# Kernel optimization log

Hardware: AMD Instinct MI355X
Metric: run time of the kernel (lower is better)

The kernel has to match this reference:

```python
import jax, jax.numpy as jnp
import numpy as np

B, L, T = 2048, 512, 32


def setup_inputs() -> dict:
    key = jax.random.key(0)
    k1, k2, k3, k4 = jax.random.split(key, 4)
    emit_score = jax.random.normal(k1, (B, L, T), dtype=jnp.float32)
    transition = jax.random.normal(k2, (T, T), dtype=jnp.float32)
    tags = jax.random.randint(k3, (B, L), 0, T, dtype=jnp.int32)
    lengths = jax.random.randint(k4, (B,), 1, L + 1, dtype=jnp.int32)
    return {"emit_score": emit_score, "transition": transition,
            "tags": tags, "lengths": lengths}


def reference(emit_score, transition, tags, lengths):
    # CRF negative log-likelihood (calculate_loss), per-example loss [B].
    b, l, t = emit_score.shape
    mask = jnp.arange(l)[None, :] < lengths[:, None]          # [B,L] bool
    maskf = mask.astype(emit_score.dtype)

    # --- gold path score ---
    gold = jnp.take_along_axis(emit_score, tags[:, :, None], axis=2)[..., 0]  # [B,L]
    trans_gold = transition[tags[:, :-1], tags[:, 1:]]        # [B,L-1]
    gold = gold.at[:, 1:].add(trans_gold)
    total_score = (gold * maskf).sum(axis=1)                  # [B]

    # --- forward algorithm (log partition) via scan over time ---
    emit_tbT = jnp.transpose(emit_score, (1, 0, 2))           # [L,B,T]
    mask_tb = mask.T                                          # [L,B]

    def step(d, x):
        e_t, m_t = x                                          # [B,T], [B]
        # scores[b, prev, next] = d[b,prev] + transition[prev,next] + e_t[b,next]
        scores = d[:, :, None] + transition[None, :, :] + e_t[:, None, :]
        new_d = jax.nn.logsumexp(scores, axis=1)              # [B,T]
        d = jnp.where(m_t[:, None], new_d, d)                 # freeze finished rows
        return d, None

    d0 = emit_tbT[0]                                          # [B,T]
    d, _ = jax.lax.scan(step, d0, (emit_tbT[1:], mask_tb[1:]))
    log_z = jax.nn.logsumexp(d, axis=1)                       # [B]

    return log_z - total_score                                # loss = -llk
```

## Files before the change

### kernel.cpp

```cpp
#include <hip/hip_runtime.h>


constexpr int TT = 32;
constexpr int LL = 512;

#define L2E  1.4426950408889634f
#define LN2f 0.6931471805599453f

template<int I>
__device__ __forceinline__ float bcastf(float v) {
  return __int_as_float(__builtin_amdgcn_ds_swizzle(__float_as_int(v), (I << 5)));
}
template<int X>
__device__ __forceinline__ float swzxf(float v) {
  return __int_as_float(__builtin_amdgcn_ds_swizzle(__float_as_int(v), (X << 10) | 0x1F));
}

__global__ __launch_bounds__(64) void crf_fwd(
    const float* __restrict__ emit, const float* __restrict__ trans,
    const int* __restrict__ tags, const int* __restrict__ lengths,
    float* __restrict__ out, int B)
{
  __shared__ float  s_trans[TT * TT];
  __shared__ float4 s_alpha[2][TT / 4];

  {
    const float4* t4 = (const float4*)trans;
    float4* st4 = (float4*)s_trans;
#pragma unroll
    for (int k = 0; k < 4; ++k)
      st4[threadIdx.x + 64 * k] = t4[threadIdx.x + 64 * k];
  }
  __syncthreads();

  const int lane = threadIdx.x & 31;
  const int grp  = threadIdx.x >> 5;
  const int b = blockIdx.x * 2 + grp;
  if (b >= B) return;
  float* sa = (float*)&s_alpha[grp][0];

  float Ec[TT];
#pragma unroll
  for (int i = 0; i < TT; ++i)
    Ec[i] = __builtin_amdgcn_exp2f(s_trans[i * TT + lane] * L2E);

  const int len = lengths[b];
  const float* erow = emit + (size_t)b * (LL * TT);
  const int*  trow  = tags + (size_t)b * LL;

  float e0   = erow[lane];
  int   ptag = trow[0];
  float a    = __builtin_amdgcn_exp2f(e0 * L2E);
  float gacc = (lane == ptag) ? e0 : 0.f;
  float LS   = 0.f;

  int mlen = max(len, __shfl_xor(len, 32));
  mlen = __builtin_amdgcn_readfirstlane(mlen);
  const int nch = (mlen - 1 + 3) >> 2;

  float eb[4], en[4];
  int   tg[4], tgn[4];
#pragma unroll
  for (int k = 0; k < 4; ++k) {
    int t = 1 + k; int tc = t < LL ? t : LL - 1;
    eb[k] = erow[tc * TT + lane];
    tg[k] = trow[tc];
  }
#pragma unroll
  for (int k = 0; k < 4; ++k) {
    int t = 5 + k; int tc = t < LL ? t : LL - 1;
    en[k] = erow[tc * TT + lane];
    tgn[k] = trow[tc];
  }

  for (int c = 0; c < nch; ++c) {
    const int tb = 1 + (c << 2);

    float ep[4]; int tgp[4];
#pragma unroll
    for (int k = 0; k < 4; ++k) {
      int t = tb + 8 + k; int tc = t < LL ? t : LL - 1;
      ep[k]  = erow[tc * TT + lane];
      tgp[k] = trow[tc];
    }

    float e2v[4];
#pragma unroll
    for (int k = 0; k < 4; ++k) e2v[k] = __builtin_amdgcn_exp2f(eb[k] * L2E);

#pragma unroll
    for (int k = 0; k < 4; ++k) {
      const int t = tb + k;

      sa[lane] = a;
      float4 A[8];
#pragma unroll
      for (int q = 0; q < 8; ++q) A[q] = s_alpha[grp][q];

      float acc0 = 0.f, acc1 = 0.f, acc2 = 0.f, acc3 = 0.f;
#pragma unroll
      for (int q = 0; q < 8; ++q) {
        acc0 = fmaf(A[q].x, Ec[4 * q + 0], acc0);
        acc1 = fmaf(A[q].y, Ec[4 * q + 1], acc1);
        acc2 = fmaf(A[q].z, Ec[4 * q + 2], acc2);
        acc3 = fmaf(A[q].w, Ec[4 * q + 3], acc3);
      }
      float anew = ((acc0 + acc1) + (acc2 + acc3)) * e2v[k];
      const bool valid = t < len;
      a = valid ? anew : a;

      int tag  = tg[k];
      float tr = s_trans[(ptag << 5) + lane];
      gacc += ((lane == tag) && valid) ? (eb[k] + tr) : 0.f;
      ptag = tag;
    }

    float m = fmaxf(bcastf<0>(a), 1e-30f);
    float r = __builtin_amdgcn_rcpf(m);
    a *= r;
    LS += __builtin_amdgcn_logf(m);

#pragma unroll
    for (int k = 0; k < 4; ++k) {
      eb[k] = en[k]; tg[k] = tgn[k];
      en[k] = ep[k]; tgn[k] = tgp[k];
    }
  }

  float s  = a;
  float gs = gacc;
  s += swzxf<1>(s);   gs += swzxf<1>(gs);
  s += swzxf<2>(s);   gs += swzxf<2>(gs);
  s += swzxf<4>(s);   gs += swzxf<4>(gs);
  s += swzxf<8>(s);   gs += swzxf<8>(gs);
  s += swzxf<16>(s);  gs += swzxf<16>(gs);

  float logz = (__builtin_amdgcn_logf(s) + LS) * LN2f;
  if (lane == 0) out[b] = logz - gs;
}

extern "C" void kernel_launch(void* const* d_in, const int* in_sizes, int n_in,
                              void* d_out, int out_size, void* d_ws, size_t ws_size,
                              hipStream_t stream) {
  const float* emit    = (const float*)d_in[0];
  const float* trans   = (const float*)d_in[1];
  const int*   tags    = (const int*)d_in[2];
  const int*   lengths = (const int*)d_in[3];
  float*       out     = (float*)d_out;
  const int B = in_sizes[3];
  const int blocks = (B + 1) / 2;
  hipLaunchKernelGGL(crf_fwd, dim3(blocks), dim3(64), 0, stream,
                     emit, trans, tags, lengths, out, B);
}
```

Measured before the change: 273.2 us.

## Split each row's 32x32 matvec across a full wave using DPP broadcasts

Each 64-lane wave now handles one sequence instead of two. Every step's 32x32 recurrence is split into 16-wide halves that are combined with permlane16/permlane32 swaps. Source values are broadcast with DPP row broadcasts, which replaces the per-step LDS store and reload of alpha. Lanes alternate between two layouts on even and odd steps, and the emission prefetch is deepened by one chunk. This shortens the serial dependency chain per timestep, at the cost of twice as many waves and more register state.

```diff
diff --git a/kernel.cpp b/kernel.cpp
--- a/kernel.cpp
+++ b/kernel.cpp
@@ -7,135 +7,174 @@
 #define L2E  1.4426950408889634f
 #define LN2f 0.6931471805599453f
 
-template<int I>
-__device__ __forceinline__ float bcastf(float v) {
-  return __int_as_float(__builtin_amdgcn_ds_swizzle(__float_as_int(v), (I << 5)));
+#define DPPBC(b, vv) __int_as_float(__builtin_amdgcn_update_dpp( \
+    0, __float_as_int(vv), 0x150 + (b), 0xF, 0xF, false))
+
+__device__ __forceinline__ float swap16(float v, int lane) {
+#if __has_builtin(__builtin_amdgcn_permlane16_swap)
+  auto p = __builtin_amdgcn_permlane16_swap(__float_as_uint(v), __float_as_uint(v),
+                                            false, false);
+  return __uint_as_float((lane & 16) ? p[0] : p[1]);
+#else
+  return __int_as_float(__builtin_amdgcn_ds_swizzle(__float_as_int(v), 0x401F));
+#endif
 }
-template<int X>
-__device__ __forceinline__ float swzxf(float v) {
-  return __int_as_float(__builtin_amdgcn_ds_swizzle(__float_as_int(v), (X << 10) | 0x1F));
+
+__device__ __forceinline__ float swap32(float v, int lane) {
+#if __has_builtin(__builtin_amdgcn_permlane32_swap)
+  auto p = __builtin_amdgcn_permlane32_swap(__float_as_uint(v), __float_as_uint(v),
+                                            false, false);
+  return __uint_as_float((lane & 32) ? p[0] : p[1]);
+#else
+  return __int_as_float(__builtin_amdgcn_ds_bpermute((lane ^ 32) << 2,
+                                                     __float_as_int(v)));
+#endif
 }
+
+#define DO_FMAS(EC) \
+  acc0 = DPPBC(0, av)  * EC[0];            \
+  acc1 = DPPBC(1, av)  * EC[1];            \
+  acc2 = DPPBC(2, av)  * EC[2];            \
+  acc3 = DPPBC(3, av)  * EC[3];            \
+  acc0 = fmaf(DPPBC(4, av),  EC[4],  acc0); \
+  acc1 = fmaf(DPPBC(5, av),  EC[5],  acc1); \
+  acc2 = fmaf(DPPBC(6, av),  EC[6],  acc2); \
+  acc3 = fmaf(DPPBC(7, av),  EC[7],  acc3); \
+  acc0 = fmaf(DPPBC(8, av),  EC[8],  acc0); \
+  acc1 = fmaf(DPPBC(9, av),  EC[9],  acc1); \
+  acc2 = fmaf(DPPBC(10, av), EC[10], acc2); \
+  acc3 = fmaf(DPPBC(11, av), EC[11], acc3); \
+  acc0 = fmaf(DPPBC(12, av), EC[12], acc0); \
+  acc1 = fmaf(DPPBC(13, av), EC[13], acc1); \
+  acc2 = fmaf(DPPBC(14, av), EC[14], acc2); \
+  acc3 = fmaf(DPPBC(15, av), EC[15], acc3);
+
+#define STEP(k, PH) do {                                            \
+    const int t = tb + (k);                                         \
+    float acc0, acc1, acc2, acc3;                                   \
+    if (PH == 0) { DO_FMAS(EcQ) } else { DO_FMAS(EcR) }             \
+    float accs = (acc0 + acc1) + (acc2 + acc3);                     \
+    float oth  = (PH == 0) ? swap16(accs, lane) : swap32(accs, lane);\
+    float sum  = accs + oth;                                        \
+    float anew = sum * e2v[k];                                      \
+    const bool valid = t < len;                                     \
+    av = valid ? anew : av;                                         \
+    int tagk = tg[k];                                               \
+    const int jc = (PH == 0) ? jcolQ : jcolR;                       \
+    float tr = s_trans[(ptag << 5) + jc];                           \
+    const bool gm = (PH == 0) ? ((lane & 16) == 0) : (lane < 32);   \
+    gacc += (valid && gm && (jc == tagk)) ? (eb[k] + tr) : 0.f;     \
+    ptag = tagk;                                                    \
+  } while (0)
 
 __global__ __launch_bounds__(64) void crf_fwd(
     const float* __restrict__ emit, const float* __restrict__ trans,
     const int* __restrict__ tags, const int* __restrict__ lengths,
     float* __restrict__ out, int B)
 {
-  __shared__ float  s_trans[TT * TT];
-  __shared__ float4 s_alpha[2][TT / 4];
-
+  __shared__ float s_trans[TT * TT];
   {
     const float4* t4 = (const float4*)trans;
-    float4* st4 = (float4*)s_trans;
+    float4* st = (float4*)s_trans;
 #pragma unroll
     for (int k = 0; k < 4; ++k)
-      st4[threadIdx.x + 64 * k] = t4[threadIdx.x + 64 * k];
+      st[threadIdx.x + 64 * k] = t4[threadIdx.x + 64 * k];
   }
   __syncthreads();
 
-  const int lane = threadIdx.x & 31;
-  const int grp  = threadIdx.x >> 5;
-  const int b = blockIdx.x * 2 + grp;
+  const int lane = threadIdx.x & 63;
+  const int j16  = lane & 15;
+  const int bit4 = (lane >> 4) & 1;
+  const int bit5 = (lane >> 5) & 1;
+  const int b = blockIdx.x;
   if (b >= B) return;
-  float* sa = (float*)&s_alpha[grp][0];
 
-  float Ec[TT];
+  const int iQ    = 16 * bit4 + j16;
+  const int jcolQ = 16 * bit5 + j16;
+  const int jcolR = 16 * bit4 + j16;
+
+  float EcQ[16], EcR[16];
 #pragma unroll
-  for (int i = 0; i < TT; ++i)
-    Ec[i] = __builtin_amdgcn_exp2f(s_trans[i * TT + lane] * L2E);
+  for (int i = 0; i < 16; ++i) {
+    EcQ[i] = __builtin_amdgcn_exp2f(s_trans[(16 * bit4 + i) * TT + jcolQ] * L2E);
+    EcR[i] = __builtin_amdgcn_exp2f(s_trans[(16 * bit5 + i) * TT + jcolR] * L2E);
+  }
 
   const int len = lengths[b];
   const float* erow = emit + (size_t)b * (LL * TT);
   const int*  trow  = tags + (size_t)b * LL;
 
-  float e0   = erow[lane];
+  float e0   = erow[iQ];
   int   ptag = trow[0];
-  float a    = __builtin_amdgcn_exp2f(e0 * L2E);
-  float gacc = (lane == ptag) ? e0 : 0.f;
+  float av   = __builtin_amdgcn_exp2f(e0 * L2E);
+  float gacc = ((lane < 32) && (iQ == ptag)) ? e0 : 0.f;
   float LS   = 0.f;
 
-  int mlen = max(len, __shfl_xor(len, 32));
-  mlen = __builtin_amdgcn_readfirstlane(mlen);
-  const int nch = (mlen - 1 + 3) >> 2;
+  const int nch = (len - 1 + 3) >> 2;
 
-  float eb[4], en[4];
-  int   tg[4], tgn[4];
+  float eb[4], en[4], ep[4];
+  int   tg[4], tgn[4], tgp[4];
 #pragma unroll
   for (int k = 0; k < 4; ++k) {
-    int t = 1 + k; int tc = t < LL ? t : LL - 1;
-    eb[k] = erow[tc * TT + lane];
+    int t = 1 + k;  int tc = t < LL ? t : LL - 1;
+    eb[k] = erow[tc * TT + ((k & 1) ? jcolR : jcolQ)];
     tg[k] = trow[tc];
   }
 #pragma unroll
   for (int k = 0; k < 4; ++k) {
-    int t = 5 + k; int tc = t < LL ? t : LL - 1;
-    en[k] = erow[tc * TT + lane];
+    int t = 5 + k;  int tc = t < LL ? t : LL - 1;
+    en[k] = erow[tc * TT + ((k & 1) ? jcolR : jcolQ)];
     tgn[k] = trow[tc];
+  }
+#pragma unroll
+  for (int k = 0; k < 4; ++k) {
+    int t = 9 + k;  int tc = t < LL ? t : LL - 1;
+    ep[k] = erow[tc * TT + ((k & 1) ? jcolR : jcolQ)];
+    tgp[k] = trow[tc];
   }
 
   for (int c = 0; c < nch; ++c) {
     const int tb = 1 + (c << 2);
 
-    float ep[4]; int tgp[4];
+    float eq[4]; int tgq[4];
 #pragma unroll
     for (int k = 0; k < 4; ++k) {
-      int t = tb + 8 + k; int tc = t < LL ? t : LL - 1;
-      ep[k]  = erow[tc * TT + lane];
-      tgp[k] = trow[tc];
+      int t = tb + 12 + k;  int tc = t < LL ? t : LL - 1;
+      eq[k]  = erow[tc * TT + ((k & 1) ? jcolR : jcolQ)];
+      tgq[k] = trow[tc];
     }
 
     float e2v[4];
 #pragma unroll
     for (int k = 0; k < 4; ++k) e2v[k] = __builtin_amdgcn_exp2f(eb[k] * L2E);
 
-#pragma unroll
-    for (int k = 0; k < 4; ++k) {
-      const int t = tb + k;
+    STEP(0, 0);
+    STEP(1, 1);
+    STEP(2, 0);
+    STEP(3, 1);
 
-      sa[lane] = a;
-      float4 A[8];
-#pragma unroll
-      for (int q = 0; q < 8; ++q) A[q] = s_alpha[grp][q];
-
-      float acc0 = 0.f, acc1 = 0.f, acc2 = 0.f, acc3 = 0.f;
-#pragma unroll
-      for (int q = 0; q < 8; ++q) {
-        acc0 = fmaf(A[q].x, Ec[4 * q + 0], acc0);
-        acc1 = fmaf(A[q].y, Ec[4 * q + 1], acc1);
-        acc2 = fmaf(A[q].z, Ec[4 * q + 2], acc2);
-        acc3 = fmaf(A[q].w, Ec[4 * q + 3], acc3);
-      }
-      float anew = ((acc0 + acc1) + (acc2 + acc3)) * e2v[k];
-      const bool valid = t < len;
-      a = valid ? anew : a;
-
-      int tag  = tg[k];
-      float tr = s_trans[(ptag << 5) + lane];
-      gacc += ((lane == tag) && valid) ? (eb[k] + tr) : 0.f;
-      ptag = tag;
-    }
-
-    float m = fmaxf(bcastf<0>(a), 1e-30f);
+    float m = __builtin_amdgcn_readfirstlane(av);
+    m = fmaxf(m, 1e-30f);
     float r = __builtin_amdgcn_rcpf(m);
-    a *= r;
+    av *= r;
     LS += __builtin_amdgcn_logf(m);
 
 #pragma unroll
     for (int k = 0; k < 4; ++k) {
-      eb[k] = en[k]; tg[k] = tgn[k];
-      en[k] = ep[k]; tgn[k] = tgp[k];
+      eb[k] = en[k];  tg[k] = tgn[k];
+      en[k] = ep[k];  tgn[k] = tgp[k];
+      ep[k] = eq[k];  tgp[k] = tgq[k];
     }
   }
 
-  float s  = a;
+  float s  = av;
   float gs = gacc;
-  s += swzxf<1>(s);   gs += swzxf<1>(gs);
-  s += swzxf<2>(s);   gs += swzxf<2>(gs);
-  s += swzxf<4>(s);   gs += swzxf<4>(gs);
-  s += swzxf<8>(s);   gs += swzxf<8>(gs);
-  s += swzxf<16>(s);  gs += swzxf<16>(gs);
-
-  float logz = (__builtin_amdgcn_logf(s) + LS) * LN2f;
+#pragma unroll
+  for (int m = 1; m <= 32; m <<= 1) {
+    s  += __shfl_xor(s, m);
+    gs += __shfl_xor(gs, m);
+  }
+  float logz = (__builtin_amdgcn_logf(s) - 1.0f + LS) * LN2f;
   if (lane == 0) out[b] = logz - gs;
 }
 
@@ -148,7 +187,6 @@
   const int*   lengths = (const int*)d_in[3];
   float*       out     = (float*)d_out;
   const int B = in_sizes[3];
-  const int blocks = (B + 1) / 2;
-  hipLaunchKernelGGL(crf_fwd, dim3(blocks), dim3(64), 0, stream,
+  hipLaunchKernelGGL(crf_fwd, dim3(B), dim3(64), 0, stream,
                      emit, trans, tags, lengths, out, B);
 }
```

New measurement: 309.8 us. +13.4%, slower.
